# Optimization experiments

Hardware: AMD Instinct MI355X
Metric: run time of the kernel (lower is better)

## Reference

```python
import jax, jax.numpy as jnp
import numpy as np

B, H, W, D, C = 1, 32, 32, 32, 256
WS = (8, 8, 8)
SS = (4, 4, 4)
NH = 8
HD = C // NH
N = WS[0] * WS[1] * WS[2]
NW = (H // WS[0]) * (W // WS[1]) * (D // WS[2])


def _rel_pos_index():
    coords = np.stack(np.meshgrid(np.arange(WS[0]), np.arange(WS[1]), np.arange(WS[2]), indexing='ij'))
    cf = coords.reshape(3, -1)
    rc = (cf[:, :, None] - cf[:, None, :]).transpose(1, 2, 0).astype(np.int64)
    rc[:, :, 0] += WS[0] - 1
    rc[:, :, 1] += WS[1] - 1
    rc[:, :, 2] += WS[2] - 1
    rc[:, :, 0] *= (2 * WS[2] - 1) * (2 * WS[1] - 1)
    rc[:, :, 1] *= (2 * WS[2] - 1)
    return rc.sum(-1).reshape(-1)  # [N*N]


def _attn_mask():
    m = np.zeros((H, W, D), np.float32)
    cnt = 0

    def sl(ws, ss):
        return ((0, -ws), (-ws, -ss), (-ss, None))

    for hs in sl(WS[0], SS[0]):
        for ws_ in sl(WS[1], SS[1]):
            for ds in sl(WS[2], SS[2]):
                m[hs[0]:hs[1], ws_[0]:ws_[1], ds[0]:ds[1]] = cnt
                cnt += 1
    m = m.reshape(H // WS[0], WS[0], W // WS[1], WS[1], D // WS[2], WS[2])
    m = m.transpose(0, 2, 4, 1, 3, 5).reshape(NW, N)
    diff = m[:, None, :] - m[:, :, None]  # [NW, N, N]
    return np.where(diff != 0, -100.0, 0.0).astype(np.float32)


REL_IDX = jnp.asarray(_rel_pos_index())
ATTN_MASK = jnp.asarray(_attn_mask())  # [NW, N, N]


def setup_inputs() -> dict:
    key = jax.random.key(0)
    ks = jax.random.split(key, 4)
    return {
        'x': jax.random.normal(ks[0], (B, H, W, D, C), jnp.float32),
        'qkv_weight': jax.random.normal(ks[1], (3 * C, C), jnp.float32) * 0.02,
        'qkv_bias': jnp.zeros((3 * C,), jnp.float32),
        'proj_weight': jax.random.normal(ks[2], (C, C), jnp.float32) * 0.02,
        'proj_bias': jnp.zeros((C,), jnp.float32),
        'rpb_table': jax.random.normal(ks[3], ((2 * WS[0] - 1) * (2 * WS[1] - 1) * (2 * WS[2] - 1), NH), jnp.float32) * 0.02,
    }


def reference(x, qkv_weight, qkv_bias, proj_weight, proj_bias, rpb_table):
    # cyclic shift
    xs = jnp.roll(x, (-SS[0], -SS[1], -SS[2]), axis=(1, 2, 3))
    # window partition -> [B*NW, N, C]
    xw = xs.reshape(B, H // WS[0], WS[0], W // WS[1], WS[1], D // WS[2], WS[2], C)
    xw = xw.transpose(0, 1, 3, 5, 2, 4, 6, 7).reshape(B * NW, N, C)
    # qkv projection
    qkv = xw @ qkv_weight.T + qkv_bias
    qkv = qkv.reshape(B * NW, N, 3, NH, HD).transpose(2, 0, 3, 1, 4)  # [3, B*NW, NH, N, HD]
    q, k, v = qkv[0] * (HD ** -0.5), qkv[1], qkv[2]
    # relative position bias [NH, N, N]
    bias = rpb_table[REL_IDX].reshape(N, N, NH).transpose(2, 0, 1)
    attn = jnp.einsum('whnd,whmd->whnm', q, k) + bias[None]
    # shift mask per window
    attn = attn.reshape(B, NW, NH, N, N) + ATTN_MASK[None, :, None]
    attn = jax.nn.softmax(attn.reshape(B * NW, NH, N, N), axis=-1)
    out = jnp.einsum('whnm,whmd->whnd', attn, v)
    out = out.transpose(0, 2, 1, 3).reshape(B * NW, N, C)
    out = out @ proj_weight.T + proj_bias
    # un-window -> [B, H, W, D, C]
    out = out.reshape(B, H // WS[0], W // WS[1], D // WS[2], WS[0], WS[1], WS[2], C)
    out = out.transpose(0, 1, 4, 2, 5, 3, 6, 7).reshape(B, H, W, D, C)
    # reverse cyclic shift
    return jnp.roll(out, (SS[0], SS[1], SS[2]), axis=(1, 2, 3))
```

## Files before the change

### kernel.cpp

```cpp
#include <hip/hip_runtime.h>

typedef __attribute__((ext_vector_type(8))) short short8;
typedef __attribute__((ext_vector_type(4))) short s4v;
typedef __attribute__((ext_vector_type(2))) uint uint2v;
typedef __attribute__((ext_vector_type(4))) uint uint4v;
typedef __attribute__((ext_vector_type(4))) float floatx4;

#define CCH   256
#define QSCALE 0.17677669529663687f
#define LOG2E  1.4426950408889634f

__device__ __forceinline__ unsigned short f2bf(float f) {
    unsigned u = __float_as_uint(f);
    u = u + 0x7fffu + ((u >> 16) & 1u);
    return (unsigned short)(u >> 16);
}

__device__ __forceinline__ uint pk2bf(float a, float b) {
    uint ua = __float_as_uint(a) + 0x8000u;
    uint ub = __float_as_uint(b) + 0x8000u;
    return __builtin_amdgcn_perm(ub, ua, 0x07060302u);
}

__device__ __forceinline__ void gl_lds16(const void* g, void* l) {
    __builtin_amdgcn_global_load_lds((const __attribute__((address_space(1))) void*)g,
                                     (__attribute__((address_space(3))) void*)l, 16, 0, 0);
}

__device__ __forceinline__ int spatial_off(int token) {
    int w = token >> 9, n = token & 511;
    int wh = w >> 4, ww = (w >> 2) & 3, wd = w & 3;
    int h1 = n >> 6, w1 = (n >> 3) & 7, d1 = n & 7;
    int gh = (wh * 8 + h1 + 4) & 31;
    int gw = (ww * 8 + w1 + 4) & 31;
    int gd = (wd * 8 + d1 + 4) & 31;
    return ((gh * 32 + gw) * 32 + gd) * CCH;
}

__global__ __launch_bounds__(256) void prep(const float* __restrict__ x,
                                            const float* __restrict__ Wq,
                                            const float* __restrict__ Wp,
                                            const float* __restrict__ rpb,
                                            ushort* __restrict__ Xw,
                                            ushort* __restrict__ Wqb,
                                            ushort* __restrict__ Wpb,
                                            uint* __restrict__ Up) {
    int b = blockIdx.x;
    if (b < 4096) {
        int tid = b * 256 + threadIdx.x;
        int token = tid >> 5, c8 = (tid & 31) * 8;
        const float* src = x + spatial_off(token) + c8;
        float4 a = *(const float4*)src;
        float4 bb = *(const float4*)(src + 4);
        uint2v lo, hi;
        lo[0] = pk2bf(a.x, a.y);
        lo[1] = pk2bf(a.z, a.w);
        hi[0] = pk2bf(bb.x, bb.y);
        hi[1] = pk2bf(bb.z, bb.w);
        uint2v* dst = (uint2v*)(Xw + (size_t)token * 256 + c8);
        dst[0] = lo;
        dst[1] = hi;
    } else if (b < 5120) {
        int tid = (b - 4096) * 256 + threadIdx.x;
        if (tid < 196608) {
            float s = (tid < 65536) ? (QSCALE * LOG2E) : 1.0f;
            Wqb[tid] = f2bf(Wq[tid] * s);
        } else {
            int i = tid - 196608;
            Wpb[i] = f2bf(Wp[i]);
        }
    } else {
        int tid = (b - 5120) * 256 + threadIdx.x;
        if (tid >= 27000) return;
        int head = tid / 3375, idx = tid - head * 3375;
        uint lo = f2bf(rpb[idx * 8 + head] * LOG2E);
        uint hi = f2bf(rpb[(idx > 0 ? idx - 1 : 0) * 8 + head] * LOG2E);
        Up[tid] = lo | (hi << 16);
    }
}

__global__ __launch_bounds__(256) void gemm_qkv(
    const ushort* __restrict__ A,
    const ushort* __restrict__ Bw,
    const float* __restrict__ bq,
    ushort* __restrict__ Q, ushort* __restrict__ K, ushort* __restrict__ Vf) {
    __shared__ short Sh[17408];
    short* As = Sh;
    short* Bs = Sh + 8192;
    const int t = threadIdx.x;
    const int wv = t >> 6, lane = t & 63, quad = lane >> 4, col = lane & 15;
    const int m0 = blockIdx.y * 128, n0 = blockIdx.x * 128;
    const int wm = (wv & 1) * 64, wn = (wv >> 1) * 64;

    floatx4 zf = {0.f, 0.f, 0.f, 0.f};
    floatx4 acc[4][4];
#pragma unroll
    for (int i = 0; i < 4; ++i)
#pragma unroll
        for (int j = 0; j < 4; ++j) acc[i][j] = zf;

    for (int kk = 0; kk < 256; kk += 64) {
        __syncthreads();
#pragma unroll
        for (int i = 0; i < 4; ++i) {
            int s = i * 256 + t;
            int row = s >> 3, qs = s & 7;
            int qg = qs ^ (row & 7);
            gl_lds16(A + (size_t)(m0 + row) * 256 + kk + qg * 8,
                     As + (i * 256 + wv * 64) * 8);
        }
#pragma unroll
        for (int i = 0; i < 4; ++i) {
            int s = i * 256 + t;
            int row = s >> 3, qs = s & 7;
            int qg = qs ^ (row & 7);
            gl_lds16(Bw + (size_t)(n0 + row) * 256 + kk + qg * 8,
                     Bs + (i * 256 + wv * 64) * 8);
        }
        __syncthreads();
#pragma unroll
        for (int h = 0; h < 2; ++h) {
            short8 af[4], bf[4];
#pragma unroll
            for (int mi = 0; mi < 4; ++mi) {
                int row = wm + mi * 16 + col;
                af[mi] = *(const short8*)(As + (row * 8 + ((h * 4 + quad) ^ (row & 7))) * 8);
            }
#pragma unroll
            for (int ni = 0; ni < 4; ++ni) {
                int row = wn + ni * 16 + col;
                bf[ni] = *(const short8*)(Bs + (row * 8 + ((h * 4 + quad) ^ (row & 7))) * 8);
            }
#pragma unroll
            for (int mi = 0; mi < 4; ++mi)
#pragma unroll
                for (int ni = 0; ni < 4; ++ni)
                    acc[mi][ni] = __builtin_amdgcn_mfma_f32_16x16x32_bf16(af[mi], bf[ni], acc[mi][ni], 0, 0, 0);
        }
    }

    const int bx = blockIdx.x;
    if (bx >= 4) {
#pragma unroll
        for (int ni = 0; ni < 4; ++ni) {
            int j = n0 + wn + ni * 16 + col;
            int head = (j >> 5) & 7, hd = j & 31;
            float bias = bq[j];
            int h = hd >> 4, colv = hd & 15;
#pragma unroll
            for (int mi = 0; mi < 4; ++mi) {
                int mb = m0 + wm + mi * 16 + quad * 4;
                int w = mb >> 9, n = mb & 511;
                size_t off = ((size_t)((w * 8 + head) * 64 + (n >> 4) * 2 + h) << 8)
                           + ((((n >> 2) & 3) * 16 + colv) << 2);
                uint2v pv;
                pv[0] = pk2bf(acc[mi][ni][0] + bias, acc[mi][ni][1] + bias);
                pv[1] = pk2bf(acc[mi][ni][2] + bias, acc[mi][ni][3] + bias);
                *(uint2v*)(Vf + off) = pv;
            }
        }
    } else {
        __syncthreads();
#pragma unroll
        for (int ni = 0; ni < 4; ++ni) {
            int j = n0 + wn + ni * 16 + col;
            int jloc = wn + ni * 16 + col;
            float bias = bq[j] * ((j < 256) ? (QSCALE * LOG2E) : 1.0f);
#pragma unroll
            for (int mi = 0; mi < 4; ++mi) {
                int rowb = wm + mi * 16 + quad * 4;
#pragma unroll
                for (int r = 0; r < 4; ++r)
                    Sh[(rowb + r) * 136 + jloc] = (short)f2bf(acc[mi][ni][r] + bias);
            }
        }
        __syncthreads();
        ushort* dst = (bx < 2) ? Q : K;
#pragma unroll
        for (int k8 = 0; k8 < 8; ++k8) {
            int chunk = k8 * 256 + t;
            int row = chunk >> 4;
            int jl = (chunk & 15) * 8;
            int j = n0 + jl;
            int m = m0 + row;
            int w = m >> 9, n = m & 511;
            int head = (j >> 5) & 7, hd = j & 31;
            uint4v vv = *(const uint4v*)(Sh + row * 136 + jl);
            size_t off;
            if (bx < 2) {
                off = ((size_t)(w * 8 + head) * 512 + n) * 32 + hd;
            } else {
                off = ((size_t)(w * 8 + head) << 14) + ((size_t)(n >> 4) << 9)
                    + (((hd >> 3) * 16 + (n & 15)) << 3);
            }
            *(uint4v*)(dst + off) = vv;
        }
    }
}

__global__ __launch_bounds__(256) void gemm_proj(
    const ushort* __restrict__ A,
    const ushort* __restrict__ Bw,
    const float* __restrict__ bp,
    float* __restrict__ out) {
    __shared__ short As[128 * 64];
    __shared__ short Bs[128 * 64];
    __shared__ float Shf[64 * 132];
    const int t = threadIdx.x;
    const int wv = t >> 6, lane = t & 63, quad = lane >> 4, col = lane & 15;
    const int m0 = blockIdx.y * 128, n0 = blockIdx.x * 128;
    const int wm = (wv & 1) * 64, wn = (wv >> 1) * 64;

    floatx4 zf = {0.f, 0.f, 0.f, 0.f};
    floatx4 acc[4][4];
#pragma unroll
    for (int i = 0; i < 4; ++i)
#pragma unroll
        for (int j = 0; j < 4; ++j) acc[i][j] = zf;

    for (int kk = 0; kk < 256; kk += 64) {
        __syncthreads();
#pragma unroll
        for (int i = 0; i < 4; ++i) {
            int s = i * 256 + t;
            int row = s >> 3, qs = s & 7;
            int qg = qs ^ (row & 7);
            gl_lds16(A + (size_t)(m0 + row) * 256 + kk + qg * 8,
                     As + (i * 256 + wv * 64) * 8);
        }
#pragma unroll
        for (int i = 0; i < 4; ++i) {
            int s = i * 256 + t;
            int row = s >> 3, qs = s & 7;
            int qg = qs ^ (row & 7);
            gl_lds16(Bw + (size_t)(n0 + row) * 256 + kk + qg * 8,
                     Bs + (i * 256 + wv * 64) * 8);
        }
        __syncthreads();
#pragma unroll
        for (int h = 0; h < 2; ++h) {
            short8 af[4], bf[4];
#pragma unroll
            for (int mi = 0; mi < 4; ++mi) {
                int row = wm + mi * 16 + col;
                af[mi] = *(const short8*)(As + (row * 8 + ((h * 4 + quad) ^ (row & 7))) * 8);
            }
#pragma unroll
            for (int ni = 0; ni < 4; ++ni) {
                int row = wn + ni * 16 + col;
                bf[ni] = *(const short8*)(Bs + (row * 8 + ((h * 4 + quad) ^ (row & 7))) * 8);
            }
#pragma unroll
            for (int mi = 0; mi < 4; ++mi)
#pragma unroll
                for (int ni = 0; ni < 4; ++ni)
                    acc[mi][ni] = __builtin_amdgcn_mfma_f32_16x16x32_bf16(af[mi], bf[ni], acc[mi][ni], 0, 0, 0);
        }
    }

    float biasv[4];
#pragma unroll
    for (int ni = 0; ni < 4; ++ni) biasv[ni] = bp[n0 + wn + ni * 16 + col];

#pragma unroll
    for (int h2 = 0; h2 < 2; ++h2) {
        __syncthreads();
        if ((wv & 1) == h2) {
#pragma unroll
            for (int ni = 0; ni < 4; ++ni) {
                int jloc = wn + ni * 16 + col;
#pragma unroll
                for (int mi = 0; mi < 4; ++mi) {
                    int rl = mi * 16 + quad * 4;
#pragma unroll
                    for (int r = 0; r < 4; ++r)
                        Shf[(rl + r) * 132 + jloc] = acc[mi][ni][r] + biasv[ni];
                }
            }
        }
        __syncthreads();
        int row = t >> 2;
        int m = m0 + h2 * 64 + row;
        float* ob = out + spatial_off(m) + n0 + (t & 3) * 4;
        const float* sb = Shf + row * 132 + (t & 3) * 4;
#pragma unroll
        for (int k = 0; k < 8; ++k)
            *(float4*)(ob + k * 16) = *(const float4*)(sb + k * 16);
    }
}

__global__ __launch_bounds__(512, 2) void attn_kernel(
    const ushort* __restrict__ Q, const ushort* __restrict__ K,
    const ushort* __restrict__ Vf, const uint* __restrict__ Up,
    ushort* __restrict__ Y) {
    __shared__ short Kl[512 * 32];
    __shared__ short Vs[64 * 256];
    __shared__ uint  Ul[3375];

    const int t = threadIdx.x;
    const int bid = blockIdx.x;
    const int w = bid >> 3, head = bid & 7;
    const int wh = w >> 4, ww = (w >> 2) & 3, wd = w & 3;
    const int wv = t >> 6, lane = t & 63, quad = lane >> 4, col = lane & 15;

    const ushort* Kg = K + (size_t)(w * 8 + head) * 512 * 32;
    const ushort* Vg = Vf + (size_t)(w * 8 + head) * 512 * 32;
    const ushort* Qg = Q + (size_t)(w * 8 + head) * 512 * 32;

#pragma unroll
    for (int i = 0; i < 4; ++i) {
        gl_lds16(Kg + (size_t)(i * 512 + t) * 8, Kl + (i * 512 + wv * 64) * 8);
        gl_lds16(Vg + (size_t)(i * 512 + t) * 8, Vs + (i * 512 + wv * 64) * 8);
    }
    const uint* Uph = Up + head * 3375;
    for (int i = t; i < 3375; i += 512) Ul[i] = Uph[i];
    __syncthreads();

    const bool boundary = (wh == 3) | (ww == 3) | (wd == 3);
    floatx4 zf = {0.f, 0.f, 0.f, 0.f};

    for (int qs = 0; qs < 4; ++qs) {
        const int qt = wv * 4 + qs;
        const short8 qf = *(const short8*)(Qg + (size_t)(qt * 16 + col) * 32 + quad * 8);

        const int qrow = qt * 16 + col;
        const int qh = qrow >> 6, qw = (qrow >> 3) & 7, qd = qrow & 7;
        const int Base0 = ((qh + 7) * 15 + (qw + 7 - (quad >> 1))) * 15
                        + (qd - ((quad & 1) << 2) + 7);
        const int cq = ((wh == 3) ? (1 + ((qrow >> 8) & 1)) * 16 : 0)
                     + ((ww == 3) ? (1 + ((qrow >> 5) & 1)) * 4 : 0)
                     + ((wd == 3) ? (1 + ((qrow >> 2) & 1)) : 0);

        float rs = 0.f;
        floatx4 o0 = zf, o1 = zf;

        for (int c = 0; c < 2; ++c) {
            const short* KlC = Kl + c * 8192;
            const short* VsC = Vs + c * 8192;
            const int BaseC = Base0 - c * 900;
            const int ckh = (wh == 3) ? ((1 + c) * 16) : 0;

            floatx4 acc[16];
#pragma unroll
            for (int tt = 0; tt < 16; ++tt) {
                const int Kt2 = ((tt >> 2) * 15 + (tt & 3) * 2) * 15;
                uint p0 = Ul[BaseC - Kt2];
                uint p1 = Ul[BaseC - Kt2 - 2];
                floatx4 cf;
                cf[0] = __uint_as_float(p0 << 16);
                cf[1] = __uint_as_float(p0 & 0xffff0000u);
                cf[2] = __uint_as_float(p1 << 16);
                cf[3] = __uint_as_float(p1 & 0xffff0000u);
                if (boundary) {
                    int ck = ckh
                           + ((ww == 3) ? (1 + ((tt >> 1) & 1)) * 4 : 0)
                           + ((wd == 3) ? (1 + (quad & 1)) : 0);
                    float madd = (cq == ck) ? 0.f : -144.269504f;
                    cf[0] += madd; cf[1] += madd; cf[2] += madd; cf[3] += madd;
                }
                short8 kf = *(const short8*)(KlC + tt * 512 + lane * 8);
                acc[tt] = __builtin_amdgcn_mfma_f32_16x16x32_bf16(kf, qf, cf, 0, 0, 0);
            }

#pragma unroll
            for (int tt = 0; tt < 16; ++tt) {
                float e0 = __builtin_amdgcn_exp2f(acc[tt][0]);
                float e1 = __builtin_amdgcn_exp2f(acc[tt][1]);
                float e2 = __builtin_amdgcn_exp2f(acc[tt][2]);
                float e3 = __builtin_amdgcn_exp2f(acc[tt][3]);
                rs += (e0 + e1) + (e2 + e3);
                uint2v pp;
                pp[0] = pk2bf(e0, e1);
                pp[1] = pk2bf(e2, e3);
                s4v pf = __builtin_bit_cast(s4v, pp);
                s4v v0 = *(const s4v*)(VsC + ((tt * 2 + 0) << 8) + lane * 4);
                s4v v1 = *(const s4v*)(VsC + ((tt * 2 + 1) << 8) + lane * 4);
                o0 = __builtin_amdgcn_mfma_f32_16x16x16bf16_1k(v0, pf, o0, 0, 0, 0);
                o1 = __builtin_amdgcn_mfma_f32_16x16x16bf16_1k(v1, pf, o1, 0, 0, 0);
            }
        }

        rs += __shfl_xor(rs, 16);
        rs += __shfl_xor(rs, 32);
        const float inv = __builtin_amdgcn_rcpf(rs);

        int token = w * 512 + qt * 16 + col;
        ushort* Yb = Y + (size_t)token * 256 + head * 32 + quad * 4;
        uint2v y0, y1;
        y0[0] = pk2bf(o0[0] * inv, o0[1] * inv);
        y0[1] = pk2bf(o0[2] * inv, o0[3] * inv);
        y1[0] = pk2bf(o1[0] * inv, o1[1] * inv);
        y1[1] = pk2bf(o1[2] * inv, o1[3] * inv);
        *(uint2v*)(Yb) = y0;
        *(uint2v*)(Yb + 16) = y1;
    }
}

extern "C" void kernel_launch(void* const* d_in, const int* in_sizes, int n_in,
                              void* d_out, int out_size, void* d_ws, size_t ws_size,
                              hipStream_t stream) {
    const float* x      = (const float*)d_in[0];
    const float* qkv_w  = (const float*)d_in[1];
    const float* qkv_b  = (const float*)d_in[2];
    const float* proj_w = (const float*)d_in[3];
    const float* proj_b = (const float*)d_in[4];
    const float* rpb    = (const float*)d_in[5];
    float* out = (float*)d_out;

    ushort* Xw  = (ushort*)d_ws;
    ushort* Q   = Xw + 8388608;
    ushort* K   = Q + 8388608;
    ushort* Vf  = K + 8388608;
    ushort* Y   = Vf + 8388608;
    uint*   Up  = (uint*)(Y + 8388608);
    ushort* Wqb = (ushort*)(Up + 27008);
    ushort* Wpb = Wqb + 196608;

    prep<<<dim3(5226), dim3(256), 0, stream>>>(x, qkv_w, proj_w, rpb, Xw, Wqb, Wpb, Up);
    gemm_qkv<<<dim3(6, 256), dim3(256), 0, stream>>>(Xw, Wqb, qkv_b, Q, K, Vf);
    attn_kernel<<<dim3(512), dim3(512), 0, stream>>>(Q, K, Vf, Up, Y);
    gemm_proj<<<dim3(2, 256), dim3(256), 0, stream>>>(Y, Wpb, proj_b, out);
}
```

Before: 171.4 us.

## Process two query tiles per pass to share K/V fragment loads

Restructures the attention inner loop so each wave handles two 16-row query tiles at once and walks keys in groups of four tiles instead of sixteen. Each K and V fragment read from LDS now feeds two MFMAs, halving LDS traffic per query tile and interleaving independent MFMA chains. The smaller groups keep the accumulator register count near the old level, but the doubled output and row-sum state may still raise register pressure and reduce occupancy.

```diff
diff --git a/kernel.cpp b/kernel.cpp
--- a/kernel.cpp
+++ b/kernel.cpp
@@ -319,80 +319,136 @@
     const bool boundary = (wh == 3) | (ww == 3) | (wd == 3);
     floatx4 zf = {0.f, 0.f, 0.f, 0.f};
 
-    for (int qs = 0; qs < 4; ++qs) {
-        const int qt = wv * 4 + qs;
-        const short8 qf = *(const short8*)(Qg + (size_t)(qt * 16 + col) * 32 + quad * 8);
-
-        const int qrow = qt * 16 + col;
-        const int qh = qrow >> 6, qw = (qrow >> 3) & 7, qd = qrow & 7;
-        const int Base0 = ((qh + 7) * 15 + (qw + 7 - (quad >> 1))) * 15
-                        + (qd - ((quad & 1) << 2) + 7);
-        const int cq = ((wh == 3) ? (1 + ((qrow >> 8) & 1)) * 16 : 0)
-                     + ((ww == 3) ? (1 + ((qrow >> 5) & 1)) * 4 : 0)
-                     + ((wd == 3) ? (1 + ((qrow >> 2) & 1)) : 0);
-
-        float rs = 0.f;
-        floatx4 o0 = zf, o1 = zf;
+    for (int qp = 0; qp < 2; ++qp) {
+        const int qtA = wv * 4 + qp * 2;
+        const int qtB = qtA + 1;
+        const short8 qfA = *(const short8*)(Qg + (size_t)(qtA * 16 + col) * 32 + quad * 8);
+        const short8 qfB = *(const short8*)(Qg + (size_t)(qtB * 16 + col) * 32 + quad * 8);
+
+        const int qrowA = qtA * 16 + col;
+        const int qrowB = qtB * 16 + col;
+        const int qhA = qrowA >> 6, qwA = (qrowA >> 3) & 7, qdA = qrowA & 7;
+        const int qhB = qrowB >> 6, qwB = (qrowB >> 3) & 7, qdB = qrowB & 7;
+        const int Base0A = ((qhA + 7) * 15 + (qwA + 7 - (quad >> 1))) * 15
+                         + (qdA - ((quad & 1) << 2) + 7);
+        const int Base0B = ((qhB + 7) * 15 + (qwB + 7 - (quad >> 1))) * 15
+                         + (qdB - ((quad & 1) << 2) + 7);
+        const int cqA = ((wh == 3) ? (1 + ((qrowA >> 8) & 1)) * 16 : 0)
+                      + ((ww == 3) ? (1 + ((qrowA >> 5) & 1)) * 4 : 0)
+                      + ((wd == 3) ? (1 + ((qrowA >> 2) & 1)) : 0);
+        const int cqB = ((wh == 3) ? (1 + ((qrowB >> 8) & 1)) * 16 : 0)
+                      + ((ww == 3) ? (1 + ((qrowB >> 5) & 1)) * 4 : 0)
+                      + ((wd == 3) ? (1 + ((qrowB >> 2) & 1)) : 0);
+
+        float rsA = 0.f, rsB = 0.f;
+        floatx4 oA0 = zf, oA1 = zf, oB0 = zf, oB1 = zf;
 
         for (int c = 0; c < 2; ++c) {
             const short* KlC = Kl + c * 8192;
             const short* VsC = Vs + c * 8192;
-            const int BaseC = Base0 - c * 900;
+            const int BaseCA = Base0A - c * 900;
+            const int BaseCB = Base0B - c * 900;
             const int ckh = (wh == 3) ? ((1 + c) * 16) : 0;
 
-            floatx4 acc[16];
-#pragma unroll
-            for (int tt = 0; tt < 16; ++tt) {
-                const int Kt2 = ((tt >> 2) * 15 + (tt & 3) * 2) * 15;
-                uint p0 = Ul[BaseC - Kt2];
-                uint p1 = Ul[BaseC - Kt2 - 2];
-                floatx4 cf;
-                cf[0] = __uint_as_float(p0 << 16);
-                cf[1] = __uint_as_float(p0 & 0xffff0000u);
-                cf[2] = __uint_as_float(p1 << 16);
-                cf[3] = __uint_as_float(p1 & 0xffff0000u);
-                if (boundary) {
-                    int ck = ckh
-                           + ((ww == 3) ? (1 + ((tt >> 1) & 1)) * 4 : 0)
-                           + ((wd == 3) ? (1 + (quad & 1)) : 0);
-                    float madd = (cq == ck) ? 0.f : -144.269504f;
-                    cf[0] += madd; cf[1] += madd; cf[2] += madd; cf[3] += madd;
+            for (int g = 0; g < 4; ++g) {
+                floatx4 accA[4], accB[4];
+#pragma unroll
+                for (int tg = 0; tg < 4; ++tg) {
+                    const int tt = g * 4 + tg;
+                    const int Kt2 = ((tt >> 2) * 15 + (tt & 3) * 2) * 15;
+                    float madd = 0.f;
+                    int ckb = 0;
+                    if (boundary) {
+                        ckb = ckh
+                            + ((ww == 3) ? (1 + ((tt >> 1) & 1)) * 4 : 0)
+                            + ((wd == 3) ? (1 + (quad & 1)) : 0);
+                    }
+                    uint p0A = Ul[BaseCA - Kt2];
+                    uint p1A = Ul[BaseCA - Kt2 - 2];
+                    floatx4 cfA;
+                    cfA[0] = __uint_as_float(p0A << 16);
+                    cfA[1] = __uint_as_float(p0A & 0xffff0000u);
+                    cfA[2] = __uint_as_float(p1A << 16);
+                    cfA[3] = __uint_as_float(p1A & 0xffff0000u);
+                    uint p0B = Ul[BaseCB - Kt2];
+                    uint p1B = Ul[BaseCB - Kt2 - 2];
+                    floatx4 cfB;
+                    cfB[0] = __uint_as_float(p0B << 16);
+                    cfB[1] = __uint_as_float(p0B & 0xffff0000u);
+                    cfB[2] = __uint_as_float(p1B << 16);
+                    cfB[3] = __uint_as_float(p1B & 0xffff0000u);
+                    if (boundary) {
+                        float mA = (cqA == ckb) ? 0.f : -144.269504f;
+                        float mB = (cqB == ckb) ? 0.f : -144.269504f;
+                        cfA[0] += mA; cfA[1] += mA; cfA[2] += mA; cfA[3] += mA;
+                        cfB[0] += mB; cfB[1] += mB; cfB[2] += mB; cfB[3] += mB;
+                    }
+                    (void)madd;
+                    short8 kf = *(const short8*)(KlC + tt * 512 + lane * 8);
+                    accA[tg] = __builtin_amdgcn_mfma_f32_16x16x32_bf16(kf, qfA, cfA, 0, 0, 0);
+                    accB[tg] = __builtin_amdgcn_mfma_f32_16x16x32_bf16(kf, qfB, cfB, 0, 0, 0);
                 }
-                short8 kf = *(const short8*)(KlC + tt * 512 + lane * 8);
-                acc[tt] = __builtin_amdgcn_mfma_f32_16x16x32_bf16(kf, qf, cf, 0, 0, 0);
-            }
-
-#pragma unroll
-            for (int tt = 0; tt < 16; ++tt) {
-                float e0 = __builtin_amdgcn_exp2f(acc[tt][0]);
-                float e1 = __builtin_amdgcn_exp2f(acc[tt][1]);
-                float e2 = __builtin_amdgcn_exp2f(acc[tt][2]);
-                float e3 = __builtin_amdgcn_exp2f(acc[tt][3]);
-                rs += (e0 + e1) + (e2 + e3);
-                uint2v pp;
-                pp[0] = pk2bf(e0, e1);
-                pp[1] = pk2bf(e2, e3);
-                s4v pf = __builtin_bit_cast(s4v, pp);
-                s4v v0 = *(const s4v*)(VsC + ((tt * 2 + 0) << 8) + lane * 4);
-                s4v v1 = *(const s4v*)(VsC + ((tt * 2 + 1) << 8) + lane * 4);
-                o0 = __builtin_amdgcn_mfma_f32_16x16x16bf16_1k(v0, pf, o0, 0, 0, 0);
-                o1 = __builtin_amdgcn_mfma_f32_16x16x16bf16_1k(v1, pf, o1, 0, 0, 0);
-            }
-        }
-
-        rs += __shfl_xor(rs, 16);
-        rs += __shfl_xor(rs, 32);
-        const float inv = __builtin_amdgcn_rcpf(rs);
-
-        int token = w * 512 + qt * 16 + col;
-        ushort* Yb = Y + (size_t)token * 256 + head * 32 + quad * 4;
-        uint2v y0, y1;
-        y0[0] = pk2bf(o0[0] * inv, o0[1] * inv);
-        y0[1] = pk2bf(o0[2] * inv, o0[3] * inv);
-        y1[0] = pk2bf(o1[0] * inv, o1[1] * inv);
-        y1[1] = pk2bf(o1[2] * inv, o1[3] * inv);
-        *(uint2v*)(Yb) = y0;
-        *(uint2v*)(Yb + 16) = y1;
+
+#pragma unroll
+                for (int tg = 0; tg < 4; ++tg) {
+                    const int tt = g * 4 + tg;
+                    float eA0 = __builtin_amdgcn_exp2f(accA[tg][0]);
+                    float eA1 = __builtin_amdgcn_exp2f(accA[tg][1]);
+                    float eA2 = __builtin_amdgcn_exp2f(accA[tg][2]);
+                    float eA3 = __builtin_amdgcn_exp2f(accA[tg][3]);
+                    rsA += (eA0 + eA1) + (eA2 + eA3);
+                    float eB0 = __builtin_amdgcn_exp2f(accB[tg][0]);
+                    float eB1 = __builtin_amdgcn_exp2f(accB[tg][1]);
+                    float eB2 = __builtin_amdgcn_exp2f(accB[tg][2]);
+                    float eB3 = __builtin_amdgcn_exp2f(accB[tg][3]);
+                    rsB += (eB0 + eB1) + (eB2 + eB3);
+                    uint2v ppA, ppB;
+                    ppA[0] = pk2bf(eA0, eA1);
+                    ppA[1] = pk2bf(eA2, eA3);
+                    ppB[0] = pk2bf(eB0, eB1);
+                    ppB[1] = pk2bf(eB2, eB3);
+                    s4v pfA = __builtin_bit_cast(s4v, ppA);
+                    s4v pfB = __builtin_bit_cast(s4v, ppB);
+                    s4v v0 = *(const s4v*)(VsC + ((tt * 2 + 0) << 8) + lane * 4);
+                    s4v v1 = *(const s4v*)(VsC + ((tt * 2 + 1) << 8) + lane * 4);
+                    oA0 = __builtin_amdgcn_mfma_f32_16x16x16bf16_1k(v0, pfA, oA0, 0, 0, 0);
+                    oB0 = __builtin_amdgcn_mfma_f32_16x16x16bf16_1k(v0, pfB, oB0, 0, 0, 0);
+                    oA1 = __builtin_amdgcn_mfma_f32_16x16x16bf16_1k(v1, pfA, oA1, 0, 0, 0);
+                    oB1 = __builtin_amdgcn_mfma_f32_16x16x16bf16_1k(v1, pfB, oB1, 0, 0, 0);
+                }
+            }
+        }
+
+        {
+            float r = rsA;
+            r += __shfl_xor(r, 16);
+            r += __shfl_xor(r, 32);
+            const float inv = __builtin_amdgcn_rcpf(r);
+            int token = w * 512 + qtA * 16 + col;
+            ushort* Yb = Y + (size_t)token * 256 + head * 32 + quad * 4;
+            uint2v y0, y1;
+            y0[0] = pk2bf(oA0[0] * inv, oA0[1] * inv);
+            y0[1] = pk2bf(oA0[2] * inv, oA0[3] * inv);
+            y1[0] = pk2bf(oA1[0] * inv, oA1[1] * inv);
+            y1[1] = pk2bf(oA1[2] * inv, oA1[3] * inv);
+            *(uint2v*)(Yb) = y0;
+            *(uint2v*)(Yb + 16) = y1;
+        }
+        {
+            float r = rsB;
+            r += __shfl_xor(r, 16);
+            r += __shfl_xor(r, 32);
+            const float inv = __builtin_amdgcn_rcpf(r);
+            int token = w * 512 + qtB * 16 + col;
+            ushort* Yb = Y + (size_t)token * 256 + head * 32 + quad * 4;
+            uint2v y0, y1;
+            y0[0] = pk2bf(oB0[0] * inv, oB0[1] * inv);
+            y0[1] = pk2bf(oB0[2] * inv, oB0[3] * inv);
+            y1[0] = pk2bf(oB1[0] * inv, oB1[1] * inv);
+            y1[1] = pk2bf(oB1[2] * inv, oB1[3] * inv);
+            *(uint2v*)(Yb) = y0;
+            *(uint2v*)(Yb + 16) = y1;
+        }
     }
 }
 
```

New measurement: 213.8 us. 1.25x slower.

## Double-buffer LDS tiles in QKV and projection GEMMs to overlap loads with MFMA

Applied to the files above, without the earlier changes.

Both GEMM kernels now use a two-stage LDS ping-pong buffer. The next K-tile's global-to-LDS copy is issued before the MFMA work on the current tile, with one barrier per iteration instead of two. The aim is to hide global load latency behind compute. In exchange, QKV GEMM shared memory grows to 64KB, which can lower occupancy, and overlap is limited because the K loop runs only four iterations.

```diff
diff --git a/kernel.cpp b/kernel.cpp
--- a/kernel.cpp
+++ b/kernel.cpp
@@ -84,9 +84,7 @@
     const ushort* __restrict__ Bw,
     const float* __restrict__ bq,
     ushort* __restrict__ Q, ushort* __restrict__ K, ushort* __restrict__ Vf) {
-    __shared__ short Sh[17408];
-    short* As = Sh;
-    short* Bs = Sh + 8192;
+    __shared__ short Sh[32768];
     const int t = threadIdx.x;
     const int wv = t >> 6, lane = t & 63, quad = lane >> 4, col = lane & 15;
     const int m0 = blockIdx.y * 128, n0 = blockIdx.x * 128;
@@ -99,25 +97,37 @@
 #pragma unroll
         for (int j = 0; j < 4; ++j) acc[i][j] = zf;
 
-    for (int kk = 0; kk < 256; kk += 64) {
-        __syncthreads();
-#pragma unroll
-        for (int i = 0; i < 4; ++i) {
-            int s = i * 256 + t;
-            int row = s >> 3, qs = s & 7;
-            int qg = qs ^ (row & 7);
-            gl_lds16(A + (size_t)(m0 + row) * 256 + kk + qg * 8,
-                     As + (i * 256 + wv * 64) * 8);
-        }
-#pragma unroll
-        for (int i = 0; i < 4; ++i) {
-            int s = i * 256 + t;
-            int row = s >> 3, qs = s & 7;
-            int qg = qs ^ (row & 7);
-            gl_lds16(Bw + (size_t)(n0 + row) * 256 + kk + qg * 8,
-                     Bs + (i * 256 + wv * 64) * 8);
-        }
-        __syncthreads();
+    const int srow = t >> 3, sqs = t & 7;
+    const int sqg = sqs ^ (srow & 7);
+
+#pragma unroll
+    for (int i = 0; i < 4; ++i) {
+        int row = (i * 256 + t) >> 3;
+        int qg = ((i * 256 + t) & 7) ^ (row & 7);
+        gl_lds16(A + (size_t)(m0 + row) * 256 + 0 + qg * 8,
+                 Sh + (i * 256 + wv * 64) * 8);
+        gl_lds16(Bw + (size_t)(n0 + row) * 256 + 0 + qg * 8,
+                 Sh + 16384 + (i * 256 + wv * 64) * 8);
+    }
+    __syncthreads();
+
+    int cur = 0;
+    for (int kt = 0; kt < 4; ++kt) {
+        int nxt = cur ^ 1;
+        if (kt < 3) {
+            int kk = (kt + 1) * 64;
+#pragma unroll
+            for (int i = 0; i < 4; ++i) {
+                int row = (i * 256 + t) >> 3;
+                int qg = ((i * 256 + t) & 7) ^ (row & 7);
+                gl_lds16(A + (size_t)(m0 + row) * 256 + kk + qg * 8,
+                         Sh + nxt * 8192 + (i * 256 + wv * 64) * 8);
+                gl_lds16(Bw + (size_t)(n0 + row) * 256 + kk + qg * 8,
+                         Sh + 16384 + nxt * 8192 + (i * 256 + wv * 64) * 8);
+            }
+        }
+        const short* As = Sh + cur * 8192;
+        const short* Bs = Sh + 16384 + cur * 8192;
 #pragma unroll
         for (int h = 0; h < 2; ++h) {
             short8 af[4], bf[4];
@@ -137,7 +147,10 @@
                 for (int ni = 0; ni < 4; ++ni)
                     acc[mi][ni] = __builtin_amdgcn_mfma_f32_16x16x32_bf16(af[mi], bf[ni], acc[mi][ni], 0, 0, 0);
         }
-    }
+        __syncthreads();
+        cur = nxt;
+    }
+    (void)srow; (void)sqg;
 
     const int bx = blockIdx.x;
     if (bx >= 4) {
@@ -184,12 +197,14 @@
             int j = n0 + jl;
             int m = m0 + row;
             int w = m >> 9, n = m & 511;
-            int head = (j >> 5) & 7, hd = j & 31;
+            int head = (j >> 5) & 7;
             uint4v vv = *(const uint4v*)(Sh + row * 136 + jl);
             size_t off;
             if (bx < 2) {
+                int hd = j & 31;
                 off = ((size_t)(w * 8 + head) * 512 + n) * 32 + hd;
             } else {
+                int hd = j & 31;
                 off = ((size_t)(w * 8 + head) << 14) + ((size_t)(n >> 4) << 9)
                     + (((hd >> 3) * 16 + (n & 15)) << 3);
             }
@@ -203,9 +218,8 @@
     const ushort* __restrict__ Bw,
     const float* __restrict__ bp,
     float* __restrict__ out) {
-    __shared__ short As[128 * 64];
-    __shared__ short Bs[128 * 64];
-    __shared__ float Shf[64 * 132];
+    __shared__ short Sh[32768];
+    float* Shf = (float*)Sh;
     const int t = threadIdx.x;
     const int wv = t >> 6, lane = t & 63, quad = lane >> 4, col = lane & 15;
     const int m0 = blockIdx.y * 128, n0 = blockIdx.x * 128;
@@ -218,25 +232,34 @@
 #pragma unroll
         for (int j = 0; j < 4; ++j) acc[i][j] = zf;
 
-    for (int kk = 0; kk < 256; kk += 64) {
-        __syncthreads();
-#pragma unroll
-        for (int i = 0; i < 4; ++i) {
-            int s = i * 256 + t;
-            int row = s >> 3, qs = s & 7;
-            int qg = qs ^ (row & 7);
-            gl_lds16(A + (size_t)(m0 + row) * 256 + kk + qg * 8,
-                     As + (i * 256 + wv * 64) * 8);
-        }
-#pragma unroll
-        for (int i = 0; i < 4; ++i) {
-            int s = i * 256 + t;
-            int row = s >> 3, qs = s & 7;
-            int qg = qs ^ (row & 7);
-            gl_lds16(Bw + (size_t)(n0 + row) * 256 + kk + qg * 8,
-                     Bs + (i * 256 + wv * 64) * 8);
-        }
-        __syncthreads();
+#pragma unroll
+    for (int i = 0; i < 4; ++i) {
+        int row = (i * 256 + t) >> 3;
+        int qg = ((i * 256 + t) & 7) ^ (row & 7);
+        gl_lds16(A + (size_t)(m0 + row) * 256 + 0 + qg * 8,
+                 Sh + (i * 256 + wv * 64) * 8);
+        gl_lds16(Bw + (size_t)(n0 + row) * 256 + 0 + qg * 8,
+                 Sh + 16384 + (i * 256 + wv * 64) * 8);
+    }
+    __syncthreads();
+
+    int cur = 0;
+    for (int kt = 0; kt < 4; ++kt) {
+        int nxt = cur ^ 1;
+        if (kt < 3) {
+            int kk = (kt + 1) * 64;
+#pragma unroll
+            for (int i = 0; i < 4; ++i) {
+                int row = (i * 256 + t) >> 3;
+                int qg = ((i * 256 + t) & 7) ^ (row & 7);
+                gl_lds16(A + (size_t)(m0 + row) * 256 + kk + qg * 8,
+                         Sh + nxt * 8192 + (i * 256 + wv * 64) * 8);
+                gl_lds16(Bw + (size_t)(n0 + row) * 256 + kk + qg * 8,
+                         Sh + 16384 + nxt * 8192 + (i * 256 + wv * 64) * 8);
+            }
+        }
+        const short* As = Sh + cur * 8192;
+        const short* Bs = Sh + 16384 + cur * 8192;
 #pragma unroll
         for (int h = 0; h < 2; ++h) {
             short8 af[4], bf[4];
@@ -256,6 +279,8 @@
                 for (int ni = 0; ni < 4; ++ni)
                     acc[mi][ni] = __builtin_amdgcn_mfma_f32_16x16x32_bf16(af[mi], bf[ni], acc[mi][ni], 0, 0, 0);
         }
+        __syncthreads();
+        cur = nxt;
     }
 
     float biasv[4];
```

Result: no change. 171.2 us (-0.1%).
